# Optimization experiments

Hardware: AMD Instinct MI355X
Metric: run time of the kernel (lower is better)

The kernel has to match this reference:

```python
import jax, jax.numpy as jnp
import numpy as np

HIDDEN = 1024
VOCAB = 128000

def setup_inputs() -> dict:
    key = jax.random.key(0)
    ks = jax.random.split(key, 9)
    s = 0.02
    return {
        "seq_input": jax.random.randint(ks[0], (1,), 0, VOCAB),
        "hidden": jax.random.normal(ks[1], (1, 1, HIDDEN), dtype=jnp.float32),
        "emb": jax.random.normal(ks[2], (VOCAB, HIDDEN), dtype=jnp.float32) * s,
        "w_ih": jax.random.normal(ks[3], (3 * HIDDEN, HIDDEN), dtype=jnp.float32) * s,
        "w_hh": jax.random.normal(ks[4], (3 * HIDDEN, HIDDEN), dtype=jnp.float32) * s,
        "b_ih": jax.random.normal(ks[5], (3 * HIDDEN,), dtype=jnp.float32) * s,
        "b_hh": jax.random.normal(ks[6], (3 * HIDDEN,), dtype=jnp.float32) * s,
        "w_out": jax.random.normal(ks[7], (VOCAB, HIDDEN), dtype=jnp.float32) * s,
        "b_out": jax.random.normal(ks[8], (VOCAB,), dtype=jnp.float32) * s,
    }

def reference(seq_input, hidden, emb, w_ih, w_hh, b_ih, b_hh, w_out, b_out):
    # embedding lookup + relu: [1, H]
    x = jax.nn.relu(emb[seq_input])
    h = hidden[0]  # [1, H] (num_layers=1, batch=1)
    # single-step GRU (PyTorch gate ordering: r, z, n)
    gi = x @ w_ih.T + b_ih     # [1, 3H]
    gh = h @ w_hh.T + b_hh     # [1, 3H]
    i_r, i_z, i_n = jnp.split(gi, 3, axis=-1)
    h_r, h_z, h_n = jnp.split(gh, 3, axis=-1)
    r = jax.nn.sigmoid(i_r + h_r)
    z = jax.nn.sigmoid(i_z + h_z)
    n = jnp.tanh(i_n + r * h_n)
    h_new = (1.0 - z) * n + z * h  # [1, H]
    # output projection + log-softmax over vocab: [1, V]
    logits = h_new @ w_out.T + b_out
    logprobs = jax.nn.log_softmax(logits, axis=1)
    return logprobs, h_new[None]  # hidden back to [1,1,H]
```

## Files before the change

kernel.cpp:

```cpp
#include <hip/hip_runtime.h>

#define H 1024
#define V 128000
#define NBLK_LOGITS 2000

#define WS_GI   0
#define WS_GH   3072
#define WS_PART 6144

__device__ __forceinline__ float wave_sum(float acc) {
    #pragma unroll
    for (int m = 32; m >= 1; m >>= 1) acc += __shfl_xor(acc, m);
    return acc;
}

__device__ __forceinline__ void online_combine(float& m, float& s, float om, float os) {
    const float M = fmaxf(m, om);
    s = s * __expf(m - M) + os * __expf(om - M);
    m = M;
}

__global__ void gates_kernel(const int* __restrict__ seq,
                             const float* __restrict__ hidden,
                             const float* __restrict__ emb,
                             const float* __restrict__ w_ih,
                             const float* __restrict__ w_hh,
                             const float* __restrict__ b_ih,
                             const float* __restrict__ b_hh,
                             float* __restrict__ ws) {
    const int wid  = threadIdx.x >> 6;
    const int lane = threadIdx.x & 63;
    const int row  = blockIdx.x * 4 + wid;
    if (row >= 6144) return;
    const int idx = seq[0];

    const float* wrow;
    const float* v;
    float bias;
    bool relu_in;
    if (row < 3072) {
        wrow = w_ih + (size_t)row * H;
        v    = emb + (size_t)idx * H;
        bias = b_ih[row];
        relu_in = true;
    } else {
        const int r = row - 3072;
        wrow = w_hh + (size_t)r * H;
        v    = hidden;
        bias = b_hh[r];
        relu_in = false;
    }

    float acc = 0.f;
    #pragma unroll
    for (int k = 0; k < 4; ++k) {
        const int j = lane * 4 + k * 256;
        float4 wv = *(const float4*)(wrow + j);
        float4 vv = *(const float4*)(v + j);
        if (relu_in) {
            vv.x = fmaxf(vv.x, 0.f); vv.y = fmaxf(vv.y, 0.f);
            vv.z = fmaxf(vv.z, 0.f); vv.w = fmaxf(vv.w, 0.f);
        }
        acc += wv.x * vv.x + wv.y * vv.y + wv.z * vv.z + wv.w * vv.w;
    }
    acc = wave_sum(acc);
    if (lane == 0) ws[row] = acc + bias;
}

__global__ void __launch_bounds__(256) logits_kernel(
        const float* __restrict__ hidden,
        const float* __restrict__ w_out,
        const float* __restrict__ b_out,
        float* __restrict__ ws,
        float* __restrict__ out) {
    __shared__ float sh_h[H];
    __shared__ float sm[4], ssum[4];
    const int tid = threadIdx.x;

    #pragma unroll
    for (int k = 0; k < 4; ++k) {
        const int i = tid + k * 256;
        const float gi_r = ws[WS_GI + i];
        const float gi_z = ws[WS_GI + H + i];
        const float gi_n = ws[WS_GI + 2 * H + i];
        const float gh_r = ws[WS_GH + i];
        const float gh_z = ws[WS_GH + H + i];
        const float gh_n = ws[WS_GH + 2 * H + i];
        const float r = 1.f / (1.f + expf(-(gi_r + gh_r)));
        const float z = 1.f / (1.f + expf(-(gi_z + gh_z)));
        const float n = tanhf(gi_n + r * gh_n);
        const float h = hidden[i];
        sh_h[i] = (1.f - z) * n + z * h;
    }
    __syncthreads();

    if (blockIdx.x == 0) {
        #pragma unroll
        for (int k = 0; k < 4; ++k) {
            const int i = tid + k * 256;
            out[V + i] = sh_h[i];
        }
    }

    const int wid  = tid >> 6;
    const int lane = tid & 63;
    float4 hv[4];
    #pragma unroll
    for (int k = 0; k < 4; ++k) hv[k] = *(const float4*)(&sh_h[lane * 4 + k * 256]);

    const int base   = blockIdx.x * 4 + wid;
    const int nwaves = NBLK_LOGITS * 4;
    float m = -1e30f, s = 0.f;
    #pragma unroll
    for (int t = 0; t < 16; t += 2) {
        const int rowA = base + t * nwaves;
        const int rowB = base + (t + 1) * nwaves;
        const float* wrA = w_out + (size_t)rowA * H;
        const float* wrB = w_out + (size_t)rowB * H;
        const float bA = b_out[rowA];
        const float bB = b_out[rowB];
        float accA = 0.f, accB = 0.f;
        #pragma unroll
        for (int k = 0; k < 4; ++k) {
            const int j = lane * 4 + k * 256;
            float4 wa = *(const float4*)(wrA + j);
            float4 wb = *(const float4*)(wrB + j);
            accA += wa.x * hv[k].x + wa.y * hv[k].y + wa.z * hv[k].z + wa.w * hv[k].w;
            accB += wb.x * hv[k].x + wb.y * hv[k].y + wb.z * hv[k].z + wb.w * hv[k].w;
        }
        #pragma unroll
        for (int d = 32; d >= 1; d >>= 1) {
            accA += __shfl_xor(accA, d);
            accB += __shfl_xor(accB, d);
        }
        accA += bA;
        accB += bB;
        if (lane == 0) { out[rowA] = accA; out[rowB] = accB; }
        float nm = fmaxf(m, accA);
        s = s * __expf(m - nm) + __expf(accA - nm);
        m = nm;
        nm = fmaxf(m, accB);
        s = s * __expf(m - nm) + __expf(accB - nm);
        m = nm;
    }

    if (lane == 0) { sm[wid] = m; ssum[wid] = s; }
    __syncthreads();
    if (tid == 0) {
        float M = sm[0], S = ssum[0];
        #pragma unroll
        for (int w = 1; w < 4; ++w) online_combine(M, S, sm[w], ssum[w]);
        ws[WS_PART + 2 * blockIdx.x]     = M;
        ws[WS_PART + 2 * blockIdx.x + 1] = S;
    }
}

__global__ void smax_write(float* __restrict__ out, const float* __restrict__ ws) {
    const int tid  = threadIdx.x;
    const int wid  = tid >> 6;
    const int lane = tid & 63;
    __shared__ float sm[4], ssum[4];
    __shared__ float c_sh;

    float m = -1e30f, s = 0.f;
    for (int i = tid; i < NBLK_LOGITS; i += 256) {
        online_combine(m, s, ws[WS_PART + 2 * i], ws[WS_PART + 2 * i + 1]);
    }
    #pragma unroll
    for (int d = 1; d < 64; d <<= 1) {
        const float om = __shfl_xor(m, d);
        const float os = __shfl_xor(s, d);
        online_combine(m, s, om, os);
    }
    if (lane == 0) { sm[wid] = m; ssum[wid] = s; }
    __syncthreads();
    if (tid == 0) {
        float M = sm[0], S = ssum[0];
        #pragma unroll
        for (int w = 1; w < 4; ++w) online_combine(M, S, sm[w], ssum[w]);
        c_sh = M + logf(S);
    }
    __syncthreads();
    const float c = c_sh;

    const int i = (blockIdx.x * 256 + tid) * 4;
    float4 v = *(float4*)(out + i);
    v.x -= c; v.y -= c; v.z -= c; v.w -= c;
    *(float4*)(out + i) = v;
}

extern "C" void kernel_launch(void* const* d_in, const int* in_sizes, int n_in,
                              void* d_out, int out_size, void* d_ws, size_t ws_size,
                              hipStream_t stream) {
    const int*   seq    = (const int*)d_in[0];
    const float* hidden = (const float*)d_in[1];
    const float* emb    = (const float*)d_in[2];
    const float* w_ih   = (const float*)d_in[3];
    const float* w_hh   = (const float*)d_in[4];
    const float* b_ih   = (const float*)d_in[5];
    const float* b_hh   = (const float*)d_in[6];
    const float* w_out  = (const float*)d_in[7];
    const float* b_out  = (const float*)d_in[8];
    float* out = (float*)d_out;
    float* ws  = (float*)d_ws;

    gates_kernel<<<1536, 256, 0, stream>>>(seq, hidden, emb, w_ih, w_hh, b_ih, b_hh, ws);
    logits_kernel<<<NBLK_LOGITS, 256, 0, stream>>>(hidden, w_out, b_out, ws, out);
    smax_write<<<125, 256, 0, stream>>>(out, ws);
}
```

Measured before the change: 109.7 us.

## Compute GRU hidden update once in last gates block via atomic counter

Moves the GRU elementwise hidden-state update out of every logits block into the final gates block, detected with an atomic completion counter. Logits blocks then just load the precomputed hidden vector from workspace. The gates grid is reshaped to 384-thread blocks covering six rows each. This removes redundant gate-combination work repeated across 2000 blocks, at the cost of a threadfence, a per-block atomic and a serialized tail block in the gates kernel.

```diff
diff --git a/kernel.cpp b/kernel.cpp
--- a/kernel.cpp
+++ b/kernel.cpp
@@ -2,17 +2,15 @@
 
 #define H 1024
 #define V 128000
+#define NBLK_GATES 1024
+#define GATES_TPB 384
 #define NBLK_LOGITS 2000
 
 #define WS_GI   0
 #define WS_GH   3072
-#define WS_PART 6144
-
-__device__ __forceinline__ float wave_sum(float acc) {
-    #pragma unroll
-    for (int m = 32; m >= 1; m >>= 1) acc += __shfl_xor(acc, m);
-    return acc;
-}
+#define WS_HN   6144
+#define WS_PART 7168
+#define WS_CNT  11168
 
 __device__ __forceinline__ void online_combine(float& m, float& s, float om, float os) {
     const float M = fmaxf(m, om);
@@ -20,19 +18,20 @@
     m = M;
 }
 
-__global__ void gates_kernel(const int* __restrict__ seq,
-                             const float* __restrict__ hidden,
-                             const float* __restrict__ emb,
-                             const float* __restrict__ w_ih,
-                             const float* __restrict__ w_hh,
-                             const float* __restrict__ b_ih,
-                             const float* __restrict__ b_hh,
-                             float* __restrict__ ws) {
+__global__ void __launch_bounds__(GATES_TPB) gates_kernel(
+        const int* __restrict__ seq,
+        const float* __restrict__ hidden,
+        const float* __restrict__ emb,
+        const float* __restrict__ w_ih,
+        const float* __restrict__ w_hh,
+        const float* __restrict__ b_ih,
+        const float* __restrict__ b_hh,
+        float* __restrict__ ws,
+        float* __restrict__ out) {
     const int wid  = threadIdx.x >> 6;
     const int lane = threadIdx.x & 63;
-    const int row  = blockIdx.x * 4 + wid;
-    if (row >= 6144) return;
-    const int idx = seq[0];
+    const int row  = blockIdx.x * 6 + wid;
+    const int idx  = seq[0];
 
     const float* wrow;
     const float* v;
@@ -63,50 +62,58 @@
         }
         acc += wv.x * vv.x + wv.y * vv.y + wv.z * vv.z + wv.w * vv.w;
     }
-    acc = wave_sum(acc);
+    #pragma unroll
+    for (int d = 32; d >= 1; d >>= 1) acc += __shfl_xor(acc, d);
     if (lane == 0) ws[row] = acc + bias;
+
+    __shared__ bool last;
+    __threadfence();
+    __syncthreads();
+    if (threadIdx.x == 0) {
+        unsigned* cnt = (unsigned*)(ws + WS_CNT);
+        unsigned old = __hip_atomic_fetch_add(cnt, 1u, __ATOMIC_ACQ_REL,
+                                              __HIP_MEMORY_SCOPE_AGENT);
+        last = ((old & (NBLK_GATES - 1)) == (NBLK_GATES - 1));
+    }
+    __syncthreads();
+    if (last) {
+        __threadfence();
+        #pragma unroll
+        for (int k = 0; k < 3; ++k) {
+            const int i = threadIdx.x + k * GATES_TPB;
+            if (i < H) {
+                const float gi_r = ws[WS_GI + i];
+                const float gi_z = ws[WS_GI + H + i];
+                const float gi_n = ws[WS_GI + 2 * H + i];
+                const float gh_r = ws[WS_GH + i];
+                const float gh_z = ws[WS_GH + H + i];
+                const float gh_n = ws[WS_GH + 2 * H + i];
+                const float r = 1.f / (1.f + expf(-(gi_r + gh_r)));
+                const float z = 1.f / (1.f + expf(-(gi_z + gh_z)));
+                const float n = tanhf(gi_n + r * gh_n);
+                const float h = hidden[i];
+                const float hn = (1.f - z) * n + z * h;
+                ws[WS_HN + i] = hn;
+                out[V + i] = hn;
+            }
+        }
+    }
 }
 
 __global__ void __launch_bounds__(256) logits_kernel(
-        const float* __restrict__ hidden,
         const float* __restrict__ w_out,
         const float* __restrict__ b_out,
         float* __restrict__ ws,
         float* __restrict__ out) {
-    __shared__ float sh_h[H];
     __shared__ float sm[4], ssum[4];
-    const int tid = threadIdx.x;
-
-    #pragma unroll
-    for (int k = 0; k < 4; ++k) {
-        const int i = tid + k * 256;
-        const float gi_r = ws[WS_GI + i];
-        const float gi_z = ws[WS_GI + H + i];
-        const float gi_n = ws[WS_GI + 2 * H + i];
-        const float gh_r = ws[WS_GH + i];
-        const float gh_z = ws[WS_GH + H + i];
-        const float gh_n = ws[WS_GH + 2 * H + i];
-        const float r = 1.f / (1.f + expf(-(gi_r + gh_r)));
-        const float z = 1.f / (1.f + expf(-(gi_z + gh_z)));
-        const float n = tanhf(gi_n + r * gh_n);
-        const float h = hidden[i];
-        sh_h[i] = (1.f - z) * n + z * h;
-    }
-    __syncthreads();
-
-    if (blockIdx.x == 0) {
-        #pragma unroll
-        for (int k = 0; k < 4; ++k) {
-            const int i = tid + k * 256;
-            out[V + i] = sh_h[i];
-        }
-    }
-
+    const int tid  = threadIdx.x;
     const int wid  = tid >> 6;
     const int lane = tid & 63;
+
     float4 hv[4];
     #pragma unroll
-    for (int k = 0; k < 4; ++k) hv[k] = *(const float4*)(&sh_h[lane * 4 + k * 256]);
+    for (int k = 0; k < 4; ++k)
+        hv[k] = *(const float4*)(ws + WS_HN + lane * 4 + k * 256);
 
     const int base   = blockIdx.x * 4 + wid;
     const int nwaves = NBLK_LOGITS * 4;
@@ -204,7 +211,8 @@
     float* out = (float*)d_out;
     float* ws  = (float*)d_ws;
 
-    gates_kernel<<<1536, 256, 0, stream>>>(seq, hidden, emb, w_ih, w_hh, b_ih, b_hh, ws);
-    logits_kernel<<<NBLK_LOGITS, 256, 0, stream>>>(hidden, w_out, b_out, ws, out);
+    gates_kernel<<<NBLK_GATES, GATES_TPB, 0, stream>>>(seq, hidden, emb, w_ih, w_hh,
+                                                       b_ih, b_hh, ws, out);
+    logits_kernel<<<NBLK_LOGITS, 256, 0, stream>>>(w_out, b_out, ws, out);
     smax_write<<<125, 256, 0, stream>>>(out, ws);
 }
```

Result: slower. 275.7 us (+151.4%).
